# Performance work log

Hardware: AMD Instinct MI355X
Metric: run time of the kernel (lower is better)

## Reference

```python
import jax, jax.numpy as jnp
import numpy as np

EMBED_DIM = 1024
NUM_HEADS = 16
HEAD_DIM = EMBED_DIM // NUM_HEADS
SCALE = HEAD_DIM ** -0.5


def setup_inputs() -> dict:
    key = jax.random.key(0)
    ks = jax.random.split(key, 12)
    B, S, D = 2, 2048, EMBED_DIM
    w_std = D ** -0.5
    return {
        "query": jax.random.normal(ks[0], (B, S, D), jnp.float32),
        "key": jax.random.normal(ks[1], (B, S, D), jnp.float32),
        "value": jax.random.normal(ks[2], (B, S, D), jnp.float32),
        "mask": jnp.ones((B, S, S), jnp.int32),
        "Wq": jax.random.normal(ks[3], (D, D), jnp.float32) * w_std,
        "bq": jnp.zeros((D,), jnp.float32),
        "Wk": jax.random.normal(ks[4], (D, D), jnp.float32) * w_std,
        "bk": jnp.zeros((D,), jnp.float32),
        "Wv": jax.random.normal(ks[5], (D, D), jnp.float32) * w_std,
        "bv": jnp.zeros((D,), jnp.float32),
        "Wo": jax.random.normal(ks[6], (D, D), jnp.float32) * w_std,
        "bo": jnp.zeros((D,), jnp.float32),
    }


def reference(query, key, value, mask, Wq, bq, Wk, bk, Wv, bv, Wo, bo):
    B, Sq, D = query.shape
    H, Hd = NUM_HEADS, HEAD_DIM
    # projections (torch Linear: x @ W.T + b), then split heads -> [B, H, S, Hd]
    q = (query @ Wq.T + bq).reshape(B, Sq, H, Hd).transpose(0, 2, 1, 3)
    k = (key @ Wk.T + bk).reshape(B, -1, H, Hd).transpose(0, 2, 1, 3)
    v = (value @ Wv.T + bv).reshape(B, -1, H, Hd).transpose(0, 2, 1, 3)
    # scaled dot-product scores [B, H, Sq, Sk]
    scores = jnp.einsum("bhqd,bhkd->bhqk", q, k) * SCALE
    scores = jnp.where(mask[:, None, :, :] == 0, -1e9, scores)
    attn_weights = jax.nn.softmax(scores, axis=-1)
    # dropout rate = 0.0 -> identity in this configuration
    attn_output = jnp.einsum("bhqk,bhkd->bhqd", attn_weights, v)
    attn_output = attn_output.transpose(0, 2, 1, 3).reshape(B, Sq, D)
    output = attn_output @ Wo.T + bo
    return (output, attn_weights)
```

## Files before the change

### kernel.cpp

```cpp
#include <hip/hip_runtime.h>
#include <stdint.h>

#define B_ 2
#define S_ 2048
#define D_ 1024
#define H_ 16
#define HD_ 64
#define NT_ (S_ / 64)
#define SC2_ 0.18033688011112042f

typedef __bf16 bf16_t;
typedef bf16_t bf16x8 __attribute__((ext_vector_type(8)));
typedef float f32x4 __attribute__((ext_vector_type(4)));
typedef unsigned short u16x8 __attribute__((ext_vector_type(8)));
typedef unsigned short u16x4 __attribute__((ext_vector_type(4)));

static __device__ __forceinline__ unsigned short f2b(float f) {
  return __builtin_bit_cast(unsigned short, (bf16_t)f);
}

static __device__ __forceinline__ bf16x8 asb(u16x8 u) {
  return __builtin_bit_cast(bf16x8, u);
}

__global__ void cast3(const float* __restrict__ a, const float* __restrict__ b,
                      const float* __restrict__ c,
                      unsigned short* __restrict__ dst, int n) {
  const float* src = blockIdx.y == 0 ? a : (blockIdx.y == 1 ? b : c);
  unsigned short* d = dst + (size_t)blockIdx.y * n;
  int i = (blockIdx.x * blockDim.x + threadIdx.x) * 8;
  if (i >= n) return;
  float4 f0 = *(const float4*)(src + i);
  float4 f1 = *(const float4*)(src + i + 4);
  u16x8 o;
  o[0] = f2b(f0.x); o[1] = f2b(f0.y); o[2] = f2b(f0.z); o[3] = f2b(f0.w);
  o[4] = f2b(f1.x); o[5] = f2b(f1.y); o[6] = f2b(f1.z); o[7] = f2b(f1.w);
  *(u16x8*)(d + i) = o;
}

__global__ void cast4(const float* __restrict__ a, const float* __restrict__ b,
                      const float* __restrict__ c, const float* __restrict__ e,
                      unsigned short* __restrict__ dst, int n) {
  const float* src = blockIdx.y == 0 ? a
                   : (blockIdx.y == 1 ? b : (blockIdx.y == 2 ? c : e));
  unsigned short* d = dst + (size_t)blockIdx.y * n;
  int i = (blockIdx.x * blockDim.x + threadIdx.x) * 8;
  if (i >= n) return;
  float4 f0 = *(const float4*)(src + i);
  float4 f1 = *(const float4*)(src + i + 4);
  u16x8 o;
  o[0] = f2b(f0.x); o[1] = f2b(f0.y); o[2] = f2b(f0.z); o[3] = f2b(f0.w);
  o[4] = f2b(f1.x); o[5] = f2b(f1.y); o[6] = f2b(f1.z); o[7] = f2b(f1.w);
  *(u16x8*)(d + i) = o;
}

__global__ void pack_mask(const int* __restrict__ mask,
                          uint32_t* __restrict__ mbits) {
  int i = blockIdx.x * blockDim.x + threadIdx.x;
  unsigned long long bits = __ballot(mask[i] != 0);
  if ((threadIdx.x & 63) == 0)
    *(unsigned long long*)&mbits[i >> 5] = bits;
}

template<int OUTMODE>
__global__ __launch_bounds__(256)
void gemm_bt(const unsigned short* __restrict__ Ab,
             const unsigned short* __restrict__ Wb,
             const float* __restrict__ bq_,
             const float* __restrict__ bk_,
             const float* __restrict__ bv_,
             void* __restrict__ outv,
             int M, int N, int K) {
  const int z = blockIdx.z;
  const unsigned short* A = Ab + (size_t)z * M * K;
  const unsigned short* W = Wb + (size_t)z * N * K;
  const float* bias = z == 0 ? bq_ : (z == 1 ? bk_ : bv_);

  __shared__ __align__(16) unsigned short As[128 * 40];
  __shared__ __align__(16) unsigned short Bs[128 * 40];

  const int tid = threadIdx.x;
  const int lane = tid & 63;
  const int wave = tid >> 6;
  const int wm = wave >> 1, wn = wave & 1;
  const int row0 = blockIdx.x * 128;
  const int col0 = blockIdx.y * 128;

  const int srow = tid >> 2;
  const int scol = (tid & 3) * 8;
  const int lr = lane & 15;
  const int lg = lane >> 4;
  const int lk = lg * 8;

  f32x4 acc[4][4] = {};

  u16x8 a0 = *(const u16x8*)&A[(size_t)(row0 + srow) * K + scol];
  u16x8 a1 = *(const u16x8*)&A[(size_t)(row0 + srow + 64) * K + scol];
  u16x8 b0 = *(const u16x8*)&W[(size_t)(col0 + srow) * K + scol];
  u16x8 b1 = *(const u16x8*)&W[(size_t)(col0 + srow + 64) * K + scol];

  for (int k0 = 0; k0 < K; k0 += 32) {
    __syncthreads();
    *(u16x8*)&As[srow * 40 + scol] = a0;
    *(u16x8*)&As[(srow + 64) * 40 + scol] = a1;
    *(u16x8*)&Bs[srow * 40 + scol] = b0;
    *(u16x8*)&Bs[(srow + 64) * 40 + scol] = b1;
    if (k0 + 32 < K) {
      a0 = *(const u16x8*)&A[(size_t)(row0 + srow) * K + k0 + 32 + scol];
      a1 = *(const u16x8*)&A[(size_t)(row0 + srow + 64) * K + k0 + 32 + scol];
      b0 = *(const u16x8*)&W[(size_t)(col0 + srow) * K + k0 + 32 + scol];
      b1 = *(const u16x8*)&W[(size_t)(col0 + srow + 64) * K + k0 + 32 + scol];
    }
    __syncthreads();

    bf16x8 af[4], bfr[4];
#pragma unroll
    for (int i = 0; i < 4; ++i)
      af[i] = asb(*(const u16x8*)&As[(wm * 64 + i * 16 + lr) * 40 + lk]);
#pragma unroll
    for (int j = 0; j < 4; ++j)
      bfr[j] = asb(*(const u16x8*)&Bs[(wn * 64 + j * 16 + lr) * 40 + lk]);
#pragma unroll
    for (int i = 0; i < 4; ++i)
#pragma unroll
      for (int j = 0; j < 4; ++j)
        acc[i][j] = __builtin_amdgcn_mfma_f32_16x16x32_bf16(af[i], bfr[j], acc[i][j], 0, 0, 0);
  }

  const size_t zo = (size_t)z * M * N;
#pragma unroll
  for (int i = 0; i < 4; ++i) {
#pragma unroll
    for (int j = 0; j < 4; ++j) {
      const int row_ = row0 + wm * 64 + i * 16 + lg * 4;
      const int col = col0 + wn * 64 + j * 16 + lr;
      const float bcol = bias[col];
      if (OUTMODE == 1) {
        float* O = (float*)outv;
#pragma unroll
        for (int r = 0; r < 4; ++r)
          __builtin_nontemporal_store(acc[i][j][r] + bcol,
                                      &O[(size_t)(row_ + r) * N + col]);
      } else if (z == 2) {
        unsigned short* O = (unsigned short*)outv + zo;
        int b = row_ >> 11, s = row_ & 2047;
        int h = col >> 6, hd = col & 63;
        u16x4 pk;
#pragma unroll
        for (int r = 0; r < 4; ++r) pk[r] = f2b(acc[i][j][r] + bcol);
        *(u16x4*)&O[(((size_t)b * H_ + h) * HD_ + hd) * S_ + s] = pk;
      } else {
        unsigned short* O = (unsigned short*)outv + zo;
        int h = col >> 6, hd = col & 63;
#pragma unroll
        for (int r = 0; r < 4; ++r) {
          int row = row_ + r;
          int b = row >> 11, s = row & 2047;
          O[(((size_t)b * H_ + h) * S_ + s) * HD_ + hd] = f2b(acc[i][j][r] + bcol);
        }
      }
    }
  }
}

static __device__ __forceinline__ void xcd_map(int& bh, int& qt) {
  int lin = blockIdx.y * 32 + blockIdx.x;
  int xcd = lin & 7, k = lin >> 3;
  bh = (xcd << 2) | (k >> 5);
  qt = k & 31;
}

__global__ __launch_bounds__(512)
void attn_pass1(const unsigned short* __restrict__ q_bh,
                const unsigned short* __restrict__ k_bh,
                const uint32_t* __restrict__ mbits,
                float2* __restrict__ ml) {
  int bh, qt;
  xcd_map(bh, qt);
  const int b = bh >> 4;
  const int q0 = qt * 64;

  __shared__ __align__(16) unsigned short Ks[64 * 72];

  const int tid = threadIdx.x, lane = tid & 63, w = tid >> 6;
  const int wq = w >> 1, wk = w & 1;
  const int srow = tid >> 3, scol = (tid & 7) * 8;
  const int lr = lane & 15, lg = lane >> 4, lk = lg * 8;
  const int sq = q0 + wq * 16 + lr;

  const unsigned short* qb = q_bh + ((size_t)bh * S_ + sq) * HD_;
  bf16x8 qf0 = asb(*(const u16x8*)&qb[lk]);
  bf16x8 qf1 = asb(*(const u16x8*)&qb[32 + lk]);

  const uint32_t* mrow = mbits + ((size_t)b * S_ + sq) * (S_ / 32);
  const unsigned short* kb = k_bh + (size_t)bh * S_ * HD_;

  float m2 = -__builtin_inff(), l = 0.f;

  u16x8 t0 = *(const u16x8*)&kb[srow * 64 + scol];

  for (int kt = 0; kt < NT_; ++kt) {
    __syncthreads();
    *(u16x8*)&Ks[srow * 72 + scol] = t0;
    if (kt + 1 < NT_) {
      const unsigned short* kn = kb + (kt + 1) * 64 * 64;
      t0 = *(const u16x8*)&kn[srow * 64 + scol];
    }
    __syncthreads();

    uint32_t mw = mrow[kt * 2 + wk];
    const bool full = __all(mw == 0xffffffffu);

    f32x4 sa[2] = {};
#pragma unroll
    for (int jj = 0; jj < 2; ++jj) {
      const int j = wk * 2 + jj;
      bf16x8 kf0 = asb(*(const u16x8*)&Ks[(j * 16 + lr) * 72 + lk]);
      bf16x8 kf1 = asb(*(const u16x8*)&Ks[(j * 16 + lr) * 72 + 32 + lk]);
      sa[jj] = __builtin_amdgcn_mfma_f32_16x16x32_bf16(kf0, qf0, sa[jj], 0, 0, 0);
      sa[jj] = __builtin_amdgcn_mfma_f32_16x16x32_bf16(kf1, qf1, sa[jj], 0, 0, 0);
    }

    float sv[2][4];
    if (full) {
#pragma unroll
      for (int jj = 0; jj < 2; ++jj)
#pragma unroll
        for (int r = 0; r < 4; ++r) sv[jj][r] = sa[jj][r] * SC2_;
    } else {
#pragma unroll
      for (int jj = 0; jj < 2; ++jj)
#pragma unroll
        for (int r = 0; r < 4; ++r) {
          int bit = jj * 16 + lg * 4 + r;
          sv[jj][r] = ((mw >> bit) & 1) ? sa[jj][r] * SC2_ : -3.0e9f;
        }
    }
    float tm = sv[0][0];
#pragma unroll
    for (int jj = 0; jj < 2; ++jj)
#pragma unroll
      for (int r = 0; r < 4; ++r) tm = fmaxf(tm, sv[jj][r]);
    tm = fmaxf(tm, __shfl_xor(tm, 16));
    tm = fmaxf(tm, __shfl_xor(tm, 32));
    float mnew = fmaxf(m2, tm);
    float ss = 0.f;
#pragma unroll
    for (int jj = 0; jj < 2; ++jj)
#pragma unroll
      for (int r = 0; r < 4; ++r)
        ss += __builtin_amdgcn_exp2f(sv[jj][r] - mnew);
    ss += __shfl_xor(ss, 16);
    ss += __shfl_xor(ss, 32);
    l = l * __builtin_amdgcn_exp2f(m2 - mnew) + ss;
    m2 = mnew;
  }

  __syncthreads();
  float2* mls = (float2*)Ks;
  if (wk == 1 && lg == 0) mls[wq * 16 + lr] = make_float2(m2, l);
  __syncthreads();
  if (wk == 0 && lg == 0) {
    float2 o = mls[wq * 16 + lr];
    float mn = fmaxf(m2, o.x);
    float lo = l * __builtin_amdgcn_exp2f(m2 - mn) +
               o.y * __builtin_amdgcn_exp2f(o.x - mn);
    ml[(size_t)bh * S_ + sq] = make_float2(mn, lo);
  }
}

__global__ __launch_bounds__(512)
void attn_pass2(const unsigned short* __restrict__ q_bh,
                const unsigned short* __restrict__ k_bh,
                const unsigned short* __restrict__ vt_g,
                const uint32_t* __restrict__ mbits,
                const float2* __restrict__ ml,
                float* __restrict__ w_out,
                unsigned short* __restrict__ attn_out) {
  int bh, qt;
  xcd_map(bh, qt);
  const int b = bh >> 4, h = bh & (H_ - 1);
  const int q0 = qt * 64;

  __shared__ __align__(16) unsigned char smem[36864];
  unsigned short* Ks = (unsigned short*)smem;
  unsigned short* Vs = Ks + 64 * 72;
  unsigned short* Ps = Vs + 64 * 72;
  float* cs = (float*)smem;

  const int tid = threadIdx.x, lane = tid & 63, w = tid >> 6;
  const int wq = w >> 1, wk = w & 1;
  const int srow = tid >> 3, scol = (tid & 7) * 8;
  const int lr = lane & 15, lg = lane >> 4, lk = lg * 8;
  const int sq = q0 + wq * 16 + lr;
  unsigned short* Psw = Ps + w * (16 * 72);

  const unsigned short* qb = q_bh + ((size_t)bh * S_ + sq) * HD_;
  bf16x8 qf0 = asb(*(const u16x8*)&qb[lk]);
  bf16x8 qf1 = asb(*(const u16x8*)&qb[32 + lk]);

  float2 t = ml[(size_t)bh * S_ + sq];
  const float off = -t.x - __builtin_amdgcn_logf(t.y);
  const uint32_t* mrow = mbits + ((size_t)b * S_ + sq) * (S_ / 32);
  float* wrow = w_out + ((size_t)bh * S_ + sq) * S_;

  const unsigned short* kb = k_bh + (size_t)bh * S_ * HD_;
  const unsigned short* vb = vt_g + (size_t)bh * HD_ * S_;

  u16x8 t0 = *(const u16x8*)&kb[srow * 64 + scol];
  u16x8 v0 = *(const u16x8*)&vb[(size_t)srow * S_ + scol];

  f32x4 oacc[4] = {};

  for (int kt = 0; kt < NT_; ++kt) {
    const int k0 = kt * 64;
    __syncthreads();
    *(u16x8*)&Ks[srow * 72 + scol] = t0;
    *(u16x8*)&Vs[srow * 72 + scol] = v0;
    if (kt + 1 < NT_) {
      t0 = *(const u16x8*)&kb[(k0 + 64 + srow) * 64 + scol];
      v0 = *(const u16x8*)&vb[(size_t)srow * S_ + k0 + 64 + scol];
    }
    __syncthreads();

    uint32_t mw = mrow[kt * 2 + wk];
    const bool full = __all(mw == 0xffffffffu);

    f32x4 sa[2] = {};
#pragma unroll
    for (int jj = 0; jj < 2; ++jj) {
      const int j = wk * 2 + jj;
      bf16x8 kf0 = asb(*(const u16x8*)&Ks[(j * 16 + lr) * 72 + lk]);
      bf16x8 kf1 = asb(*(const u16x8*)&Ks[(j * 16 + lr) * 72 + 32 + lk]);
      sa[jj] = __builtin_amdgcn_mfma_f32_16x16x32_bf16(kf0, qf0, sa[jj], 0, 0, 0);
      sa[jj] = __builtin_amdgcn_mfma_f32_16x16x32_bf16(kf1, qf1, sa[jj], 0, 0, 0);
    }

#pragma unroll
    for (int jj = 0; jj < 2; ++jj) {
      f32x4 pv;
      u16x4 pb;
      if (full) {
#pragma unroll
        for (int r = 0; r < 4; ++r) {
          float p = __builtin_amdgcn_exp2f(fmaf(sa[jj][r], SC2_, off));
          pv[r] = p;
          pb[r] = f2b(p);
        }
      } else {
#pragma unroll
        for (int r = 0; r < 4; ++r) {
          int bit = jj * 16 + lg * 4 + r;
          float x = ((mw >> bit) & 1) ? fmaf(sa[jj][r], SC2_, off) : -3.0e9f;
          float p = __builtin_amdgcn_exp2f(x);
          pv[r] = p;
          pb[r] = f2b(p);
        }
      }
      __builtin_nontemporal_store(pv,
          (f32x4*)&wrow[k0 + wk * 32 + jj * 16 + lg * 4]);
      *(u16x4*)&Psw[lr * 72 + wk * 32 + jj * 16 + lg * 4] = pb;
    }

    bf16x8 pa = asb(*(const u16x8*)&Psw[lr * 72 + wk * 32 + lk]);
#pragma unroll
    for (int j2 = 0; j2 < 4; ++j2) {
      bf16x8 vf = asb(*(const u16x8*)&Vs[(j2 * 16 + lr) * 72 + wk * 32 + lk]);
      oacc[j2] = __builtin_amdgcn_mfma_f32_16x16x32_bf16(pa, vf, oacc[j2], 0, 0, 0);
    }
  }

  __syncthreads();
  const int ci = (wq * 64 + lane) * 17;
  if (wk == 1) {
#pragma unroll
    for (int j2 = 0; j2 < 4; ++j2)
#pragma unroll
      for (int r = 0; r < 4; ++r) cs[ci + j2 * 4 + r] = oacc[j2][r];
  }
  __syncthreads();
  if (wk == 0) {
#pragma unroll
    for (int j2 = 0; j2 < 4; ++j2)
#pragma unroll
      for (int r = 0; r < 4; ++r) {
        float v = oacc[j2][r] + cs[ci + j2 * 4 + r];
        attn_out[((size_t)b * S_ + q0 + wq * 16 + lg * 4 + r) * D_ + h * HD_ + j2 * 16 + lr] =
            f2b(v);
      }
  }
}

extern "C" void kernel_launch(void* const* d_in, const int* in_sizes, int n_in,
                              void* d_out, int out_size, void* d_ws, size_t ws_size,
                              hipStream_t stream) {
  const float* query = (const float*)d_in[0];
  const float* key   = (const float*)d_in[1];
  const float* value = (const float*)d_in[2];
  const int*   mask  = (const int*)d_in[3];
  const float* Wq = (const float*)d_in[4];
  const float* bq = (const float*)d_in[5];
  const float* Wk = (const float*)d_in[6];
  const float* bk = (const float*)d_in[7];
  const float* Wv = (const float*)d_in[8];
  const float* bv = (const float*)d_in[9];
  const float* Wo = (const float*)d_in[10];
  const float* bo = (const float*)d_in[11];

  const int NE = B_ * S_ * D_;
  const int NW = D_ * D_;

  char* ws = (char*)d_ws;
  unsigned short* xin  = (unsigned short*)(ws);
  uint32_t*       mbits = (uint32_t*)(ws + 8388608);
  unsigned short* wbuf = (unsigned short*)(ws + 25165824);
  unsigned short* qkv  = (unsigned short*)(ws + 33554432);
  float2* mlbuf        = (float2*)(ws + 58720256);
  unsigned short* aout = (unsigned short*)(ws + 59244544);

  cast3<<<dim3(NE / 2048, 3), dim3(256), 0, stream>>>(query, key, value, xin, NE);
  cast4<<<dim3(NW / 2048, 4), dim3(256), 0, stream>>>(Wq, Wk, Wv, Wo, wbuf, NW);

  gemm_bt<0><<<dim3(32, 8, 3), dim3(256), 0, stream>>>(
      xin, wbuf, bq, bk, bv, qkv, 4096, 1024, 1024);

  pack_mask<<<dim3(B_ * S_ * S_ / 256), dim3(256), 0, stream>>>(mask, mbits);

  float* w_out = (float*)d_out + NE;
  attn_pass1<<<dim3(32, 32), dim3(512), 0, stream>>>(qkv, qkv + NE, mbits, mlbuf);
  attn_pass2<<<dim3(32, 32), dim3(512), 0, stream>>>(
      qkv, qkv + NE, qkv + 2 * NE, mbits, mlbuf, w_out, aout);

  gemm_bt<1><<<dim3(32, 8, 1), dim3(256), 0, stream>>>(
      aout, wbuf + 3 * NW, bo, bo, bo, d_out, 4096, 1024, 1024);
}
```

Measured before the change: 297.5 us.

## Load GEMM tiles directly into LDS with global_load_lds

The projection GEMM now copies its A and W tiles straight from global memory into shared memory with the global_load_lds builtin, instead of staging them through registers. This drops the padded 40-element row stride for an unpadded 32, as the direct-to-LDS path writes contiguous rows. It removes the register prefetch, so the load for the next k-step no longer overlaps with the MFMA work of the current one. The unpadded layout may also bring LDS bank conflicts on fragment reads.

```diff
diff --git a/kernel.cpp b/kernel.cpp
--- a/kernel.cpp
+++ b/kernel.cpp
@@ -21,6 +21,13 @@
 
 static __device__ __forceinline__ bf16x8 asb(u16x8 u) {
   return __builtin_bit_cast(bf16x8, u);
+}
+
+static __device__ __forceinline__ void gload16(const unsigned short* g,
+                                               unsigned short* l) {
+  __builtin_amdgcn_global_load_lds(
+      (const __attribute__((address_space(1))) void*)g,
+      (__attribute__((address_space(3))) void*)l, 16, 0, 0);
 }
 
 __global__ void cast3(const float* __restrict__ a, const float* __restrict__ b,
@@ -76,8 +83,8 @@
   const unsigned short* W = Wb + (size_t)z * N * K;
   const float* bias = z == 0 ? bq_ : (z == 1 ? bk_ : bv_);
 
-  __shared__ __align__(16) unsigned short As[128 * 40];
-  __shared__ __align__(16) unsigned short Bs[128 * 40];
+  __shared__ __align__(16) unsigned short As[128 * 32];
+  __shared__ __align__(16) unsigned short Bs[128 * 32];
 
   const int tid = threadIdx.x;
   const int lane = tid & 63;
@@ -86,40 +93,38 @@
   const int row0 = blockIdx.x * 128;
   const int col0 = blockIdx.y * 128;
 
-  const int srow = tid >> 2;
-  const int scol = (tid & 3) * 8;
   const int lr = lane & 15;
   const int lg = lane >> 4;
   const int lk = lg * 8;
 
+  const int srow = wave * 16 + (lane >> 2);
+  const int scol = (lane & 3) * 8;
+  const unsigned short* a_src0 = &A[(size_t)(row0 + srow) * K + scol];
+  const unsigned short* a_src1 = &A[(size_t)(row0 + 64 + srow) * K + scol];
+  const unsigned short* b_src0 = &W[(size_t)(col0 + srow) * K + scol];
+  const unsigned short* b_src1 = &W[(size_t)(col0 + 64 + srow) * K + scol];
+  unsigned short* a_dst0 = &As[(wave * 16) * 32];
+  unsigned short* a_dst1 = &As[(64 + wave * 16) * 32];
+  unsigned short* b_dst0 = &Bs[(wave * 16) * 32];
+  unsigned short* b_dst1 = &Bs[(64 + wave * 16) * 32];
+
   f32x4 acc[4][4] = {};
 
-  u16x8 a0 = *(const u16x8*)&A[(size_t)(row0 + srow) * K + scol];
-  u16x8 a1 = *(const u16x8*)&A[(size_t)(row0 + srow + 64) * K + scol];
-  u16x8 b0 = *(const u16x8*)&W[(size_t)(col0 + srow) * K + scol];
-  u16x8 b1 = *(const u16x8*)&W[(size_t)(col0 + srow + 64) * K + scol];
-
   for (int k0 = 0; k0 < K; k0 += 32) {
     __syncthreads();
-    *(u16x8*)&As[srow * 40 + scol] = a0;
-    *(u16x8*)&As[(srow + 64) * 40 + scol] = a1;
-    *(u16x8*)&Bs[srow * 40 + scol] = b0;
-    *(u16x8*)&Bs[(srow + 64) * 40 + scol] = b1;
-    if (k0 + 32 < K) {
-      a0 = *(const u16x8*)&A[(size_t)(row0 + srow) * K + k0 + 32 + scol];
-      a1 = *(const u16x8*)&A[(size_t)(row0 + srow + 64) * K + k0 + 32 + scol];
-      b0 = *(const u16x8*)&W[(size_t)(col0 + srow) * K + k0 + 32 + scol];
-      b1 = *(const u16x8*)&W[(size_t)(col0 + srow + 64) * K + k0 + 32 + scol];
-    }
+    gload16(a_src0 + k0, a_dst0);
+    gload16(a_src1 + k0, a_dst1);
+    gload16(b_src0 + k0, b_dst0);
+    gload16(b_src1 + k0, b_dst1);
     __syncthreads();
 
     bf16x8 af[4], bfr[4];
 #pragma unroll
     for (int i = 0; i < 4; ++i)
-      af[i] = asb(*(const u16x8*)&As[(wm * 64 + i * 16 + lr) * 40 + lk]);
+      af[i] = asb(*(const u16x8*)&As[(wm * 64 + i * 16 + lr) * 32 + lk]);
 #pragma unroll
     for (int j = 0; j < 4; ++j)
-      bfr[j] = asb(*(const u16x8*)&Bs[(wn * 64 + j * 16 + lr) * 40 + lk]);
+      bfr[j] = asb(*(const u16x8*)&Bs[(wn * 64 + j * 16 + lr) * 32 + lk]);
 #pragma unroll
     for (int i = 0; i < 4; ++i)
 #pragma unroll
```

Result: slower. 305.6 us (+2.7%).
